# Optimization experiments

Hardware: AMD Instinct MI355X
Metric: run time of the kernel (lower is better)

## Reference

```python
import jax, jax.numpy as jnp
import numpy as np

B, H, W, C = 8, 28, 28, 1024
NH = 16
HD = C // NH
HID = 4 * C
BC = C // 2
SCALE = HD ** -0.5
EPS_LN = 1e-5   # nn.LayerNorm default
EPS_CLN = 1e-6  # detectron2 LayerNorm default


def layer_norm(x, w, b, eps=EPS_LN):
    m = jnp.mean(x, -1, keepdims=True)
    v = jnp.mean((x - m) ** 2, -1, keepdims=True)
    return (x - m) * jax.lax.rsqrt(v + eps) * w + b


def conv2d(x, w, padding):
    return jax.lax.conv_general_dilated(x, w, (1, 1), padding,
                                        dimension_numbers=("NHWC", "HWIO", "NHWC"))


def rel_table(rel_pos, size):
    # q_size == k_size, so relative index is simply (i - j) + (size - 1)
    idx = jnp.arange(size)[:, None] - jnp.arange(size)[None, :] + (size - 1)
    return rel_pos[idx]  # (size, size, HD)


def setup_inputs() -> dict:
    key = jax.random.key(0)
    ks = jax.random.split(key, 12)
    rn = lambda k, shape, s=0.02: jax.random.normal(k, shape, jnp.float32) * s
    return {
        "x": jax.random.normal(ks[0], (B, H, W, C), jnp.float32),
        "ln1_w": jnp.ones((C,), jnp.float32), "ln1_b": jnp.zeros((C,), jnp.float32),
        "qkv_w": rn(ks[1], (C, 3 * C)), "qkv_b": jnp.zeros((3 * C,), jnp.float32),
        "proj_w": rn(ks[2], (C, C)), "proj_b": jnp.zeros((C,), jnp.float32),
        "rel_pos_h": rn(ks[3], (2 * H - 1, HD)),
        "rel_pos_w": rn(ks[4], (2 * W - 1, HD)),
        "ln2_w": jnp.ones((C,), jnp.float32), "ln2_b": jnp.zeros((C,), jnp.float32),
        "mlp_w1": rn(ks[5], (C, HID)), "mlp_b1": jnp.zeros((HID,), jnp.float32),
        "mlp_w2": rn(ks[6], (HID, C)), "mlp_b2": jnp.zeros((C,), jnp.float32),
        "conv1_w": rn(ks[7], (1, 1, C, BC)),
        "cln1_w": jnp.ones((BC,), jnp.float32), "cln1_b": jnp.zeros((BC,), jnp.float32),
        "conv2_w": rn(ks[8], (3, 3, BC, BC)),
        "cln2_w": jnp.ones((BC,), jnp.float32), "cln2_b": jnp.zeros((BC,), jnp.float32),
        "conv3_w": rn(ks[9], (1, 1, BC, C)),
        "cln3_w": jnp.ones((C,), jnp.float32), "cln3_b": jnp.zeros((C,), jnp.float32),
    }


def _attention(h, qkv_w, qkv_b, proj_w, proj_b, rel_pos_h, rel_pos_w):
    # h: (B, N, C) with N = H*W
    Bq, N, _ = h.shape
    qkv = (h @ qkv_w + qkv_b).reshape(Bq, N, 3, NH, HD)
    q, k, v = jnp.moveaxis(qkv, 2, 0)          # each (B, N, NH, HD)
    q = jnp.swapaxes(q, 1, 2)                  # (B, NH, N, HD)
    k = jnp.swapaxes(k, 1, 2)
    v = jnp.swapaxes(v, 1, 2)
    attn = jnp.einsum("bhqd,bhkd->bhqk", q * SCALE, k)  # (B, NH, N, N)
    # decomposed relative position bias (uses UNscaled q, as in torch source)
    Rh = rel_table(rel_pos_h, H)               # (H, H, HD)
    Rw = rel_table(rel_pos_w, W)               # (W, W, HD)
    rq = q.reshape(Bq, NH, H, W, HD)
    rel_h = jnp.einsum("bnhwd,hkd->bnhwk", rq, Rh)  # (B, NH, H, W, H)
    rel_w = jnp.einsum("bnhwd,wkd->bnhwk", rq, Rw)  # (B, NH, H, W, W)
    attn = (attn.reshape(Bq, NH, H, W, H, W)
            + rel_h[..., :, None] + rel_w[..., None, :]).reshape(Bq, NH, N, N)
    attn = jax.nn.softmax(attn, axis=-1)
    out = jnp.einsum("bhqk,bhkd->bhqd", attn, v)     # (B, NH, N, HD)
    out = jnp.swapaxes(out, 1, 2).reshape(Bq, N, C)
    return out @ proj_w + proj_b


def reference(x, ln1_w, ln1_b, qkv_w, qkv_b, proj_w, proj_b, rel_pos_h, rel_pos_w,
              ln2_w, ln2_b, mlp_w1, mlp_b1, mlp_w2, mlp_b2,
              conv1_w, cln1_w, cln1_b, conv2_w, cln2_w, cln2_b,
              conv3_w, cln3_w, cln3_b):
    Bq = x.shape[0]
    N = H * W
    xt = x.reshape(Bq, N, C)
    shortcut = xt
    h = layer_norm(xt, ln1_w, ln1_b)
    a = _attention(h, qkv_w, qkv_b, proj_w, proj_b, rel_pos_h, rel_pos_w)
    xt = shortcut + a
    h2 = layer_norm(xt, ln2_w, ln2_b)
    mlp = jax.nn.gelu(h2 @ mlp_w1 + mlp_b1, approximate=False) @ mlp_w2 + mlp_b2
    xt = xt + mlp
    y = xt.reshape(Bq, H, W, C)
    # residual bottleneck conv block (NHWC; detectron2 LN == per-pixel channel LN)
    o = conv2d(y, conv1_w, "VALID")
    o = jax.nn.gelu(layer_norm(o, cln1_w, cln1_b, EPS_CLN), approximate=False)
    o = conv2d(o, conv2_w, "SAME")
    o = jax.nn.gelu(layer_norm(o, cln2_w, cln2_b, EPS_CLN), approximate=False)
    o = conv2d(o, conv3_w, "VALID")
    o = layer_norm(o, cln3_w, cln3_b, EPS_CLN)
    return y + o
```

## Files before the change

kernel.cpp:

```cpp
#include <hip/hip_runtime.h>
#include <hip/hip_bf16.h>

#define DI __device__ __forceinline__

typedef short bf16x8 __attribute__((ext_vector_type(8)));
typedef float f32x4 __attribute__((ext_vector_type(4)));

constexpr int BB = 8, CC = 1024, NHEAD = 16, HD = 64, HIDC = 4096, BCC = 512;
constexpr int NT = 784;
constexpr int MROWS = BB * NT;
constexpr float ATT_SCALE = 0.125f;

DI short f2bf(float f) {
    unsigned u = __builtin_bit_cast(unsigned, f);
    u = u + 0x7FFFu + ((u >> 16) & 1u);
    return (short)(u >> 16);
}
DI float bf2f(short h) {
    unsigned u = ((unsigned)(unsigned short)h) << 16;
    return __builtin_bit_cast(float, u);
}
DI float gelu_f(float x) { return 0.5f * x * (1.0f + erff(x * 0.70710678118654752f)); }

DI void gload16(const void* g, void* l) {
    __builtin_amdgcn_global_load_lds(
        (const __attribute__((address_space(1))) void*)g,
        (__attribute__((address_space(3))) void*)l, 16, 0, 0);
}

__global__ __launch_bounds__(256)
void cvt_t_kernel(const float* __restrict__ in, short* __restrict__ out, int K, int N) {
    __shared__ short t[64][68];
    const int k0 = blockIdx.y * 64, n0 = blockIdx.x * 64;
    const int tid = threadIdx.x;
    const int r = tid >> 4, c4 = (tid & 15) << 2;
    #pragma unroll
    for (int rr = 0; rr < 64; rr += 16) {
        float4 v = *(const float4*)(in + (size_t)(k0 + r + rr) * N + n0 + c4);
        t[r + rr][c4 + 0] = f2bf(v.x); t[r + rr][c4 + 1] = f2bf(v.y);
        t[r + rr][c4 + 2] = f2bf(v.z); t[r + rr][c4 + 3] = f2bf(v.w);
    }
    __syncthreads();
    #pragma unroll
    for (int rr = 0; rr < 64; rr += 16) {
        int nrow = r + rr;
        short4 o;
        o.x = t[c4 + 0][nrow]; o.y = t[c4 + 1][nrow];
        o.z = t[c4 + 2][nrow]; o.w = t[c4 + 3][nrow];
        *(short4*)(out + (size_t)(n0 + nrow) * K + k0 + c4) = o;
    }
}

__global__ void cvt_tables_kernel(const float* __restrict__ rph, const float* __restrict__ rpw,
                                  short* __restrict__ rhb, short* __restrict__ rwb) {
    int i = blockIdx.x * 256 + threadIdx.x;
    if (i < 3520) rhb[i] = f2bf(rph[i]);
    else if (i < 7040) rwb[i - 3520] = f2bf(rpw[i - 3520]);
}

template<bool GELU_, bool RESID, bool OUTBF>
__global__ void ln_kernel(const float* __restrict__ in, const float* __restrict__ gw,
                          const float* __restrict__ gb, const float* __restrict__ resid,
                          void* __restrict__ outv, int C, float eps) {
    const int row = blockIdx.x;
    const int tid = threadIdx.x;
    const float* x = in + (size_t)row * C;
    const int c4 = C >> 2;
    float s = 0.f, s2 = 0.f;
    for (int i = tid; i < c4; i += 256) {
        float4 v = ((const float4*)x)[i];
        s += v.x + v.y + v.z + v.w;
        s2 += v.x * v.x + v.y * v.y + v.z * v.z + v.w * v.w;
    }
    for (int off = 32; off; off >>= 1) { s += __shfl_xor(s, off); s2 += __shfl_xor(s2, off); }
    __shared__ float sa[4], sb[4], stats[2];
    int wid = tid >> 6;
    if ((tid & 63) == 0) { sa[wid] = s; sb[wid] = s2; }
    __syncthreads();
    if (tid == 0) {
        float S = sa[0] + sa[1] + sa[2] + sa[3];
        float S2 = sb[0] + sb[1] + sb[2] + sb[3];
        float mean = S / C;
        float var = S2 / C - mean * mean;
        stats[0] = mean; stats[1] = rsqrtf(var + eps);
    }
    __syncthreads();
    const float mean = stats[0], rstd = stats[1];
    for (int i = tid; i < c4; i += 256) {
        float4 v = ((const float4*)x)[i];
        float4 w4 = ((const float4*)gw)[i];
        float4 b4 = ((const float4*)gb)[i];
        float o[4] = { (v.x - mean) * rstd * w4.x + b4.x,
                       (v.y - mean) * rstd * w4.y + b4.y,
                       (v.z - mean) * rstd * w4.z + b4.z,
                       (v.w - mean) * rstd * w4.w + b4.w };
        if (GELU_) {
            #pragma unroll
            for (int j = 0; j < 4; j++) o[j] = gelu_f(o[j]);
        }
        if (RESID) {
            float4 r4 = ((const float4*)(resid + (size_t)row * C))[i];
            o[0] += r4.x; o[1] += r4.y; o[2] += r4.z; o[3] += r4.w;
        }
        if (OUTBF) {
            short4 ov; ov.x = f2bf(o[0]); ov.y = f2bf(o[1]); ov.z = f2bf(o[2]); ov.w = f2bf(o[3]);
            ((short4*)((short*)outv + (size_t)row * C))[i] = ov;
        } else {
            float4 ov; ov.x = o[0]; ov.y = o[1]; ov.z = o[2]; ov.w = o[3];
            ((float4*)((float*)outv + (size_t)row * C))[i] = ov;
        }
    }
}

template<bool OUTBF, bool HASB, bool ACTG, bool HASR, bool IMC, bool DUAL>
__global__ __launch_bounds__(256)
void gemm_kernel(const short* __restrict__ A, const short* __restrict__ Bt,
                 const float* __restrict__ bias, const float* __restrict__ resid,
                 void* __restrict__ outv, short* __restrict__ out2,
                 int M, int N, int K, const short* __restrict__ zg) {
    __shared__ __align__(16) short As[2 * 128 * 32];
    __shared__ __align__(16) short Bs[2 * 128 * 32];
    const int tid = threadIdx.x;
    const int nwg = gridDim.x * gridDim.y;
    const int orig = blockIdx.y * gridDim.x + blockIdx.x;
    const int qq = nwg >> 3, rr8 = nwg & 7;
    const int xcd = orig & 7, loc = orig >> 3;
    const int wg = (xcd < rr8 ? xcd * (qq + 1) : rr8 * (qq + 1) + (xcd - rr8) * qq) + loc;
    const int m0 = (wg / gridDim.x) * 128, n0 = (wg % gridDim.x) * 128;
    const int lane = tid & 63, wid = tid >> 6;
    const int wr = (wid >> 1) * 64, wc = (wid & 1) * 64;
    const int lr = lane & 15, lkb = lane >> 4;

    const int srow = lane >> 2;
    const int schunk = lane & 3;

    const short* aptr[2];
    const short* bptr[2];
    int sdst[2];
    int ihh[2], iww[2], ioff[2];
    const short* ibase[2];

    #pragma unroll
    for (int i = 0; i < 2; i++) {
        int seg = wid * 2 + i;
        int row = seg * 16 + srow;
        int c = schunk ^ (row & 3);
        sdst[i] = seg * 512;
        bptr[i] = Bt + (size_t)(n0 + row) * K + c * 8;
        if (!IMC) {
            aptr[i] = A + (size_t)(m0 + row) * K + c * 8;
        } else {
            int m = m0 + row;
            int bimg = m / 784, rem = m - bimg * 784;
            ihh[i] = rem / 28; iww[i] = rem - (rem / 28) * 28;
            ibase[i] = A + (size_t)bimg * 784 * 512;
            ioff[i] = c * 8;
        }
    }

    auto stage = [&](int kt, int buf) {
        short* ab = As + buf * 4096;
        short* bb = Bs + buf * 4096;
        if (!IMC) {
            #pragma unroll
            for (int i = 0; i < 2; i++) {
                gload16(aptr[i] + kt * 32, ab + sdst[i]);
                gload16(bptr[i] + kt * 32, bb + sdst[i]);
            }
        } else {
            int segk = kt >> 4;
            int ky = segk / 3, kx = segk - ky * 3;
            int ccb = (kt & 15) << 5;
            #pragma unroll
            for (int i = 0; i < 2; i++) {
                int ih = ihh[i] + ky - 1, iw = iww[i] + kx - 1;
                bool ok = (ih >= 0) & (ih < 28) & (iw >= 0) & (iw < 28);
                const short* s = ok ? ibase[i] + ((size_t)(ih * 28 + iw) * 512 + ccb + ioff[i]) : zg;
                gload16(s, ab + sdst[i]);
                gload16(bptr[i] + kt * 32, bb + sdst[i]);
            }
        }
    };

    f32x4 acc[4][4];
    #pragma unroll
    for (int i = 0; i < 4; i++)
        #pragma unroll
        for (int j = 0; j < 4; j++) acc[i][j] = f32x4{0.f, 0.f, 0.f, 0.f};

    const int pc = (lkb ^ (lr & 3)) << 3;
    const int nkt = K >> 5;
    int cur = 0;
    stage(0, 0);
    for (int kt = 0; kt < nkt; ++kt) {
        if (kt + 1 < nkt) {
            stage(kt + 1, cur ^ 1);
            asm volatile("s_waitcnt vmcnt(4)" ::: "memory");
        } else {
            asm volatile("s_waitcnt vmcnt(0)" ::: "memory");
        }
        __builtin_amdgcn_sched_barrier(0);
        __builtin_amdgcn_s_barrier();
        __builtin_amdgcn_sched_barrier(0);
        const short* ab = As + cur * 4096;
        const short* bb = Bs + cur * 4096;
        bf16x8 af[4], bfv[4];
        #pragma unroll
        for (int mt = 0; mt < 4; mt++) af[mt] = *(const bf16x8*)&ab[(wr + mt * 16 + lr) * 32 + pc];
        #pragma unroll
        for (int nt = 0; nt < 4; nt++) bfv[nt] = *(const bf16x8*)&bb[(wc + nt * 16 + lr) * 32 + pc];
        #pragma unroll
        for (int mt = 0; mt < 4; mt++)
            #pragma unroll
            for (int nt = 0; nt < 4; nt++)
                acc[mt][nt] = __builtin_amdgcn_mfma_f32_16x16x32_bf16(af[mt], bfv[nt], acc[mt][nt], 0, 0, 0);
        __builtin_amdgcn_s_barrier();
        __builtin_amdgcn_sched_barrier(0);
        cur ^= 1;
    }
    const int ro = (lane >> 4) << 2;
    #pragma unroll
    for (int mt = 0; mt < 4; mt++) {
        #pragma unroll
        for (int nt = 0; nt < 4; nt++) {
            int col = n0 + wc + nt * 16 + lr;
            float bv = HASB ? bias[col] : 0.0f;
            #pragma unroll
            for (int j = 0; j < 4; j++) {
                int row = m0 + wr + mt * 16 + ro + j;
                float v = acc[mt][nt][j] + bv;
                if (ACTG) v = gelu_f(v);
                size_t oi = (size_t)row * N + col;
                if (HASR) v += resid[oi];
                if (OUTBF) ((short*)outv)[oi] = f2bf(v);
                else       ((float*)outv)[oi] = v;
                if (DUAL)  out2[oi] = f2bf(v);
            }
        }
    }
}

__global__ __launch_bounds__(64)
void relpos_mfma_kernel(const short* __restrict__ qkv, const short* __restrict__ rhb,
                        const short* __restrict__ rwb, float* __restrict__ relh,
                        float* __restrict__ relw) {
    const int p = blockIdx.x;
    const int bh = blockIdx.y;
    const int mode = blockIdx.z;
    const int bimg = bh >> 4, nh = bh & 15;
    const int lane = threadIdx.x;
    const int lr = lane & 15, lkb = lane >> 4;
    const short* rb = mode ? rwb : rhb;
    float* outp = mode ? relw : relh;

    bf16x8 afr[2][2];
    #pragma unroll
    for (int mt = 0; mt < 2; mt++) {
        int kh = mt * 16 + lr;
        int sr = p - kh + 27;
        sr = sr < 0 ? 0 : (sr > 54 ? 54 : sr);
        #pragma unroll
        for (int ks = 0; ks < 2; ks++)
            afr[mt][ks] = *(const bf16x8*)(rb + sr * 64 + ks * 32 + lkb * 8);
    }
    bf16x8 bfq[2][2];
    #pragma unroll
    for (int nt = 0; nt < 2; nt++) {
        int cc = nt * 16 + lr;
        int nlin = mode ? (cc * 28 + p) : (p * 28 + cc);
        if (nlin > 783) nlin = 783;
        const short* qp = qkv + (size_t)(bimg * 784 + nlin) * 3072 + nh * 64;
        #pragma unroll
        for (int ks = 0; ks < 2; ks++)
            bfq[nt][ks] = *(const bf16x8*)(qp + ks * 32 + lkb * 8);
    }
    f32x4 acc[2][2];
    #pragma unroll
    for (int i = 0; i < 2; i++)
        #pragma unroll
        for (int j = 0; j < 2; j++) acc[i][j] = f32x4{0.f, 0.f, 0.f, 0.f};
    #pragma unroll
    for (int ks = 0; ks < 2; ks++)
        #pragma unroll
        for (int mt = 0; mt < 2; mt++)
            #pragma unroll
            for (int nt = 0; nt < 2; nt++)
                acc[mt][nt] = __builtin_amdgcn_mfma_f32_16x16x32_bf16(afr[mt][ks], bfq[nt][ks], acc[mt][nt], 0, 0, 0);
    const int ro = lkb << 2;
    #pragma unroll
    for (int nt = 0; nt < 2; nt++) {
        int cc = nt * 16 + lr;
        if (cc < 28) {
            int nlin = mode ? (cc * 28 + p) : (p * 28 + cc);
            float* o = outp + ((size_t)bh * 784 + nlin) * 28;
            *(f32x4*)(o + ro) = acc[0][nt];
            if (ro < 12) *(f32x4*)(o + 16 + ro) = acc[1][nt];
        }
    }
}

__global__ __launch_bounds__(256)
void attn_kernel(const short* __restrict__ qkv, const float* __restrict__ relh,
                 const float* __restrict__ relw, short* __restrict__ outp) {
    constexpr int VSTR = 34;
    __shared__ __align__(16) short Ks[32 * 64];
    __shared__ __align__(16) short Vt[64 * VSTR];
    __shared__ __align__(16) short Pl[4][16 * 40];
    __shared__ float relS[4][16 * 57];
    const int qb = blockIdx.x;
    const int bh = blockIdx.y;
    const int bimg = bh >> 4, nh = bh & 15;
    const int tid = threadIdx.x;
    const int lane = tid & 63, wid = tid >> 6;
    const int lr = lane & 15, lkb = lane >> 4;
    const int lk = lkb * 8;
    const int qw0 = qb * 64 + wid * 16;

    for (int idx = lane; idx < 16 * 56; idx += 64) {
        int qq = idx / 56, j = idx - qq * 56;
        int n = qw0 + qq; if (n > 783) n = 783;
        relS[wid][qq * 57 + j] = (j < 28) ? relh[((size_t)bh * 784 + n) * 28 + j]
                                          : relw[((size_t)bh * 784 + n) * 28 + (j - 28)];
    }
    bf16x8 bq0, bq1;
    {
        int tok = qw0 + lr; if (tok > 783) tok = 783;
        const short* qp = qkv + (size_t)(bimg * 784 + tok) * 3072 + nh * 64;
        bq0 = *(const bf16x8*)(qp + lk);
        bq1 = *(const bf16x8*)(qp + 32 + lk);
    }
    f32x4 oacc[4];
    #pragma unroll
    for (int i = 0; i < 4; i++) oacc[i] = f32x4{0.f, 0.f, 0.f, 0.f};
    float m_run = -1e30f, l_run = 0.0f;

    const int krow = tid >> 3, kcp = tid & 7;
    const int kclog = kcp ^ (krow & 7);
    short* kdst = Ks + wid * 512;
    const int vkey = tid & 31, vdb = tid >> 5;
    const int kq4 = lkb << 2;

    for (int kt = 0; kt < 25; ++kt) {
        const int k0 = kt * 32;
        {
            int key = k0 + krow; if (key > 783) key = 783;
            gload16(qkv + (size_t)(bimg * 784 + key) * 3072 + 1024 + nh * 64 + kclog * 8, kdst);
        }
        {
            int key = k0 + vkey; if (key > 783) key = 783;
            bf16x8 vv = *(const bf16x8*)(qkv + (size_t)(bimg * 784 + key) * 3072 + 2048 + nh * 64 + vdb * 8);
            #pragma unroll
            for (int j = 0; j < 8; j++) Vt[(vdb * 8 + j) * VSTR + vkey] = vv[j];
        }
        __syncthreads();
        f32x4 sacc[2];
        sacc[0] = f32x4{0.f, 0.f, 0.f, 0.f}; sacc[1] = f32x4{0.f, 0.f, 0.f, 0.f};
        #pragma unroll
        for (int mb = 0; mb < 2; mb++) {
            int row = mb * 16 + lr;
            bf16x8 ak0 = *(const bf16x8*)&Ks[row * 64 + ((lkb ^ (row & 7)) << 3)];
            bf16x8 ak1 = *(const bf16x8*)&Ks[row * 64 + (((4 + lkb) ^ (row & 7)) << 3)];
            sacc[mb] = __builtin_amdgcn_mfma_f32_16x16x32_bf16(ak0, bq0, sacc[mb], 0, 0, 0);
            sacc[mb] = __builtin_amdgcn_mfma_f32_16x16x32_bf16(ak1, bq1, sacc[mb], 0, 0, 0);
        }
        float sv[8];
        #pragma unroll
        for (int mb = 0; mb < 2; mb++)
            #pragma unroll
            for (int j = 0; j < 4; j++) {
                int key = k0 + mb * 16 + kq4 + j;
                float v;
                if (key < 784) {
                    int h2 = key / 28, w2 = key - (key / 28) * 28;
                    v = sacc[mb][j] * ATT_SCALE + relS[wid][lr * 57 + h2] + relS[wid][lr * 57 + 28 + w2];
                } else v = -1e30f;
                sv[mb * 4 + j] = v;
            }
        float mt_ = sv[0];
        #pragma unroll
        for (int i = 1; i < 8; i++) mt_ = fmaxf(mt_, sv[i]);
        mt_ = fmaxf(mt_, __shfl_xor(mt_, 16));
        mt_ = fmaxf(mt_, __shfl_xor(mt_, 32));
        if (__all(mt_ - m_run <= 8.0f)) {
            float psum = 0.f;
            #pragma unroll
            for (int i = 0; i < 8; i++) {
                float pz = __expf(sv[i] - m_run);
                psum += pz;
                Pl[wid][lr * 40 + ((i >> 2) * 16 + kq4 + (i & 3))] = f2bf(pz);
            }
            psum += __shfl_xor(psum, 16);
            psum += __shfl_xor(psum, 32);
            l_run += psum;
        } else {
            float mnew = fmaxf(m_run, mt_);
            float corr = __expf(m_run - mnew);
            float psum = 0.f;
            #pragma unroll
            for (int i = 0; i < 8; i++) {
                float pz = __expf(sv[i] - mnew);
                psum += pz;
                Pl[wid][lr * 40 + ((i >> 2) * 16 + kq4 + (i & 3))] = f2bf(pz);
            }
            psum += __shfl_xor(psum, 16);
            psum += __shfl_xor(psum, 32);
            l_run = l_run * corr + psum;
            m_run = mnew;
            #pragma unroll
            for (int db = 0; db < 4; db++) {
                f32x4 t = oacc[db];
                t[0] *= corr; t[1] *= corr; t[2] *= corr; t[3] *= corr;
                oacc[db] = t;
            }
        }
        bf16x8 pb = *(const bf16x8*)&Pl[wid][lr * 40 + lk];
        #pragma unroll
        for (int db = 0; db < 4; db++) {
            bf16x8 av = *(const bf16x8*)&Vt[(db * 16 + lr) * VSTR + lk];
            oacc[db] = __builtin_amdgcn_mfma_f32_16x16x32_bf16(av, pb, oacc[db], 0, 0, 0);
        }
        __syncthreads();
    }
    const float inv = 1.0f / l_run;
    const int tok = qw0 + lr;
    if (tok < 784) {
        short* op = outp + (size_t)(bimg * 784 + tok) * 1024 + nh * 64;
        #pragma unroll
        for (int db = 0; db < 4; db++)
            #pragma unroll
            for (int j = 0; j < 4; j++) {
                int d = db * 16 + kq4 + j;
                op[d] = f2bf(oacc[db][j] * inv);
            }
    }
}

extern "C" void kernel_launch(void* const* d_in, const int* in_sizes, int n_in,
                              void* d_out, int out_size, void* d_ws, size_t ws_size,
                              hipStream_t stream) {
    const float* x      = (const float*)d_in[0];
    const float* ln1w   = (const float*)d_in[1];
    const float* ln1b   = (const float*)d_in[2];
    const float* qkvw   = (const float*)d_in[3];
    const float* qkvbia = (const float*)d_in[4];
    const float* projw  = (const float*)d_in[5];
    const float* projb  = (const float*)d_in[6];
    const float* rph    = (const float*)d_in[7];
    const float* rpw    = (const float*)d_in[8];
    const float* ln2w   = (const float*)d_in[9];
    const float* ln2b   = (const float*)d_in[10];
    const float* m1w    = (const float*)d_in[11];
    const float* m1b    = (const float*)d_in[12];
    const float* m2w    = (const float*)d_in[13];
    const float* m2b    = (const float*)d_in[14];
    const float* c1w    = (const float*)d_in[15];
    const float* cl1w   = (const float*)d_in[16];
    const float* cl1b   = (const float*)d_in[17];
    const float* c2w    = (const float*)d_in[18];
    const float* cl2w   = (const float*)d_in[19];
    const float* cl2b   = (const float*)d_in[20];
    const float* c3w    = (const float*)d_in[21];
    const float* cl3w   = (const float*)d_in[22];
    const float* cl3b   = (const float*)d_in[23];
    float* out = (float*)d_out;

    char* base = (char*)d_ws;
    size_t off = 0;
    auto alloc = [&](size_t bytes) -> char* {
        char* p = base + off;
        off = (off + bytes + 255) & ~(size_t)255;
        return p;
    };
    short* wq  = (short*)alloc((size_t)3072 * 1024 * 2);
    short* wp  = (short*)alloc((size_t)1024 * 1024 * 2);
    short* w1  = (short*)alloc((size_t)4096 * 1024 * 2);
    short* w2  = (short*)alloc((size_t)1024 * 4096 * 2);
    short* wc1 = (short*)alloc((size_t)512 * 1024 * 2);
    short* wc2 = (short*)alloc((size_t)512 * 4608 * 2);
    short* wc3 = (short*)alloc((size_t)1024 * 512 * 2);
    short* hbuf = (short*)alloc((size_t)MROWS * 1024 * 2);
    short* qkvb = (short*)alloc((size_t)MROWS * 3072 * 2);
    float* relh = (float*)alloc((size_t)128 * 784 * 28 * 4);
    float* relw = (float*)alloc((size_t)128 * 784 * 28 * 4);
    float* xt   = (float*)alloc((size_t)MROWS * 1024 * 4);
    short* hid  = (short*)alloc((size_t)MROWS * 4096 * 2);
    float* yf   = (float*)alloc((size_t)MROWS * 1024 * 4);
    short* zg   = (short*)alloc(256);
    short* rhb  = (short*)alloc(3520 * 2);
    short* rwb  = (short*)alloc(3520 * 2);
    (void)relw; (void)ws_size; (void)in_sizes; (void)n_in; (void)out_size;

    float* o1f  = (float*)hid;
    short* o1g  = (short*)((char*)hid + (size_t)MROWS * 512 * 4);
    float* o2f  = (float*)((char*)o1g + (size_t)MROWS * 512 * 2);
    short* o2g  = (short*)((char*)o2f + (size_t)MROWS * 512 * 4);
    float* o3f  = (float*)qkvb;
    short* ybf  = (short*)relh;

    hipMemsetAsync(zg, 0, 256, stream);

    auto cvtT = [&](const float* src, short* dst, int K, int N) {
        cvt_t_kernel<<<dim3(N / 64, K / 64), 256, 0, stream>>>(src, dst, K, N);
    };
    cvtT(qkvw, wq, 1024, 3072);
    cvtT(projw, wp, 1024, 1024);
    cvtT(m1w, w1, 1024, 4096);
    cvtT(m2w, w2, 4096, 1024);
    cvtT(c1w, wc1, 1024, 512);
    cvtT(c2w, wc2, 4608, 512);
    cvtT(c3w, wc3, 512, 1024);
    cvt_tables_kernel<<<28, 256, 0, stream>>>(rph, rpw, rhb, rwb);

    ln_kernel<false, false, true><<<MROWS, 256, 0, stream>>>(x, ln1w, ln1b, nullptr, hbuf, 1024, 1e-5f);
    gemm_kernel<true, true, false, false, false, false><<<dim3(24, 49), 256, 0, stream>>>(
        hbuf, wq, qkvbia, nullptr, qkvb, nullptr, MROWS, 3072, 1024, zg);
    relpos_mfma_kernel<<<dim3(28, 128, 2), 64, 0, stream>>>(qkvb, rhb, rwb, relh, relw);
    attn_kernel<<<dim3(13, 128), 256, 0, stream>>>(qkvb, relh, relw, hbuf);
    gemm_kernel<false, true, false, true, false, false><<<dim3(8, 49), 256, 0, stream>>>(
        hbuf, wp, projb, x, xt, nullptr, MROWS, 1024, 1024, zg);
    ln_kernel<false, false, true><<<MROWS, 256, 0, stream>>>(xt, ln2w, ln2b, nullptr, hbuf, 1024, 1e-5f);
    gemm_kernel<true, true, true, false, false, false><<<dim3(32, 49), 256, 0, stream>>>(
        hbuf, w1, m1b, nullptr, hid, nullptr, MROWS, 4096, 1024, zg);
    gemm_kernel<false, true, false, true, false, true><<<dim3(8, 49), 256, 0, stream>>>(
        hid, w2, m2b, xt, yf, ybf, MROWS, 1024, 4096, zg);
    gemm_kernel<false, false, false, false, false, false><<<dim3(4, 49), 256, 0, stream>>>(
        ybf, wc1, nullptr, nullptr, o1f, nullptr, MROWS, 512, 1024, zg);
    ln_kernel<true, false, true><<<MROWS, 256, 0, stream>>>(o1f, cl1w, cl1b, nullptr, o1g, 512, 1e-6f);
    gemm_kernel<false, false, false, false, true, false><<<dim3(4, 49), 256, 0, stream>>>(
        o1g, wc2, nullptr, nullptr, o2f, nullptr, MROWS, 512, 4608, zg);
    ln_kernel<true, false, true><<<MROWS, 256, 0, stream>>>(o2f, cl2w, cl2b, nullptr, o2g, 512, 1e-6f);
    gemm_kernel<false, false, false, false, false, false><<<dim3(8, 49), 256, 0, stream>>>(
        o2g, wc3, nullptr, nullptr, o3f, nullptr, MROWS, 1024, 512, zg);
    ln_kernel<false, true, false><<<MROWS, 256, 0, stream>>>(o3f, cl3w, cl3b, yf, out, 1024, 1e-6f);
}
```

Measured before the change: 731.9 us.

## Deepen GEMM LDS pipeline to four stages with one barrier per iteration

Replaces the double-buffered LDS staging in the GEMM kernel with a four-slot ring that keeps three K-tiles of global loads in flight, and drops the trailing barrier in each iteration. The aim is to hide more global-memory latency and cut barrier overhead in every GEMM, including the implicit-im2col conv. LDS use per block doubles to 64KB, which can lower occupancy. Correctness depends on the slot-reuse distance keeping a slot from being overwritten while another wave is still reading it.

```diff
diff --git a/kernel.cpp b/kernel.cpp
--- a/kernel.cpp
+++ b/kernel.cpp
@@ -118,8 +118,8 @@
                  const float* __restrict__ bias, const float* __restrict__ resid,
                  void* __restrict__ outv, short* __restrict__ out2,
                  int M, int N, int K, const short* __restrict__ zg) {
-    __shared__ __align__(16) short As[2 * 128 * 32];
-    __shared__ __align__(16) short Bs[2 * 128 * 32];
+    __shared__ __align__(16) short As[4][128 * 32];
+    __shared__ __align__(16) short Bs[4][128 * 32];
     const int tid = threadIdx.x;
     const int nwg = gridDim.x * gridDim.y;
     const int orig = blockIdx.y * gridDim.x + blockIdx.x;
@@ -158,9 +158,10 @@
         }
     }
 
-    auto stage = [&](int kt, int buf) {
-        short* ab = As + buf * 4096;
-        short* bb = Bs + buf * 4096;
+    auto stage = [&](int kt) {
+        const int slot = kt & 3;
+        short* ab = &As[slot][0];
+        short* bb = &Bs[slot][0];
         if (!IMC) {
             #pragma unroll
             for (int i = 0; i < 2; i++) {
@@ -190,20 +191,18 @@
 
     const int pc = (lkb ^ (lr & 3)) << 3;
     const int nkt = K >> 5;
-    int cur = 0;
-    stage(0, 0);
+
+    stage(0); stage(1); stage(2);
     for (int kt = 0; kt < nkt; ++kt) {
-        if (kt + 1 < nkt) {
-            stage(kt + 1, cur ^ 1);
-            asm volatile("s_waitcnt vmcnt(4)" ::: "memory");
-        } else {
-            asm volatile("s_waitcnt vmcnt(0)" ::: "memory");
-        }
+        if (kt < nkt - 2)       asm volatile("s_waitcnt vmcnt(8)" ::: "memory");
+        else if (kt == nkt - 2) asm volatile("s_waitcnt vmcnt(4)" ::: "memory");
+        else                    asm volatile("s_waitcnt vmcnt(0)" ::: "memory");
         __builtin_amdgcn_sched_barrier(0);
         __builtin_amdgcn_s_barrier();
         __builtin_amdgcn_sched_barrier(0);
-        const short* ab = As + cur * 4096;
-        const short* bb = Bs + cur * 4096;
+        if (kt + 3 < nkt) stage(kt + 3);
+        const short* ab = &As[kt & 3][0];
+        const short* bb = &Bs[kt & 3][0];
         bf16x8 af[4], bfv[4];
         #pragma unroll
         for (int mt = 0; mt < 4; mt++) af[mt] = *(const bf16x8*)&ab[(wr + mt * 16 + lr) * 32 + pc];
@@ -214,9 +213,6 @@
             #pragma unroll
             for (int nt = 0; nt < 4; nt++)
                 acc[mt][nt] = __builtin_amdgcn_mfma_f32_16x16x32_bf16(af[mt], bfv[nt], acc[mt][nt], 0, 0, 0);
-        __builtin_amdgcn_s_barrier();
-        __builtin_amdgcn_sched_barrier(0);
-        cur ^= 1;
     }
     const int ro = (lane >> 4) << 2;
     #pragma unroll
```

Result: slower. 807.4 us (+10.3%).
